# Kernel tuning notes

Measured on AMD Instinct MI355X. Metric: run time of the kernel, lower is better.

## Reference

```python
import jax, jax.numpy as jnp
import numpy as np

B, T, C = 4, 4096, 1024
NH, DH = 16, 128          # n_head, d_head = d_qkv // n_head
DQKV, DR = 2048, 256      # d_qkv, d_rank


def _uniform(key, shape, bound):
    return jax.random.uniform(key, shape, jnp.float32, -bound, bound)


def setup_inputs() -> dict:
    key = jax.random.key(0)
    k0, k1, k2, k3, k4 = jax.random.split(key, 5)
    # CastedLinear init: bound = sqrt(3) * 0.5 * in_features**-0.5 (same for w1, w2)
    b_qkv = (3 ** 0.5) * 0.5 * C ** (-0.5)
    b_proj = (3 ** 0.5) * 0.5 * DQKV ** (-0.5)
    return {
        "x": jax.random.normal(k0, (B, T, C), jnp.float32),
        "qkv_w1": _uniform(k1, (DR, C), b_qkv),
        "qkv_w2": _uniform(k2, (3 * DQKV, DR), b_qkv),
        "cproj_w1": _uniform(k3, (DR, DQKV), b_proj),
        "cproj_w2": _uniform(k4, (2 * C, DR), b_proj),
    }


def _rmsnorm(x):
    eps = jnp.finfo(x.dtype).eps  # F.rms_norm default eps
    return x * jax.lax.rsqrt(jnp.mean(x * x, axis=-1, keepdims=True) + eps)


def reference(x, qkv_w1, qkv_w2, cproj_w1, cproj_w2):
    Bx, Tx, Cx = x.shape
    # qkv projection with low-rank factorization + relu^2 activation between factors
    h = _rmsnorm(x) @ qkv_w1.T                      # [B,T,DR]
    h = jnp.square(jax.nn.relu(h))
    qkv = (h @ qkv_w2.T).reshape(Bx, Tx, 3 * NH, DH)
    q, k, v = jnp.split(qkv, 3, axis=2)             # each [B,T,NH,DH]
    q, k = _rmsnorm(q), _rmsnorm(k)

    # rotary embedding: half the head dim rotated, second quarter frequencies zero
    quarter = DH // 4
    freq = (1.0 / 1024.0) ** jnp.linspace(0.0, 1.0, quarter)
    freq = jnp.concatenate([freq, jnp.zeros(quarter, freq.dtype)])  # [DH//2]
    theta = jnp.arange(Tx, dtype=jnp.float32)[:, None] * freq[None, :]
    cos = jnp.cos(theta)[None, :, None, :]          # [1,T,1,DH//2]
    sin = jnp.sin(theta)[None, :, None, :]

    def rope(z):
        z1, z2 = jnp.split(z, 2, axis=-1)
        return jnp.concatenate([z1 * cos + z2 * sin, -z1 * sin + z2 * cos], axis=-1)

    q, k = rope(q), rope(k)

    # causal linear attention: sigmoid-gated cumulative sum over time
    y = jax.nn.relu(q) * jnp.cumsum(jax.nn.sigmoid(k) * v, axis=1)  # [B,T,NH,DH]
    y = y.reshape(Bx, Tx, NH * DH)

    # low-rank output projection (no activation), gated residual
    uv = (y @ cproj_w1.T) @ cproj_w2.T              # [B,T,2C]
    u, g = jnp.split(uv, 2, axis=-1)
    return x + u * jax.nn.silu(g)
```

## Files before the change

### kernel.cpp

```cpp
#include <hip/hip_runtime.h>
#include <hip/hip_bf16.h>

#define TB 4
#define TT 4096
#define TC 1024
#define TNH 16
#define TDH 128
#define TDQKV 2048
#define TDR 256
#define RB 4096
#define ROWS (TB*TT)
#define SLAB (RB*128)

typedef __attribute__((ext_vector_type(8))) short bfx8;
typedef __attribute__((ext_vector_type(4))) float fx4;
typedef __attribute__((address_space(1))) const unsigned char GAS;
typedef __attribute__((address_space(3))) unsigned char LAS;

__device__ __forceinline__ unsigned short f2b(float f) {
    unsigned int u = __float_as_uint(f);
    unsigned int r = (u + 0x7fffu + ((u >> 16) & 1u)) >> 16;
    return (unsigned short)r;
}
__device__ __forceinline__ float b2f(unsigned short h) {
    return __uint_as_float(((unsigned int)h) << 16);
}
__device__ __forceinline__ float sigm(float x) {
    return 1.0f / (1.0f + __expf(-x));
}
__device__ __forceinline__ int xcd_swz(int hw, int nwg) {
    int q = nwg >> 3;
    return (hw & 7) * q + (hw >> 3);
}

__global__ __launch_bounds__(256) void cvt_bf16(const float* __restrict__ in,
                                                unsigned short* __restrict__ out, int n) {
    int i = (blockIdx.x * 256 + threadIdx.x) * 4;
    if (i < n) {
        float4 v = *(const float4*)(in + i);
        out[i + 0] = f2b(v.x);
        out[i + 1] = f2b(v.y);
        out[i + 2] = f2b(v.z);
        out[i + 3] = f2b(v.w);
    }
}

__global__ __launch_bounds__(256) void rope_tab(float* __restrict__ ct, float* __restrict__ st) {
    int i = blockIdx.x * 256 + threadIdx.x;
    int t = i >> 5, j = i & 31;
    float fr = exp2f(-10.0f * (float)j / 31.0f);
    float th = (float)t * fr;
    ct[i] = cosf(th);
    st[i] = sinf(th);
}

__global__ __launch_bounds__(256) void rmsnorm_x(const float* __restrict__ x,
                                                 unsigned short* __restrict__ xn) {
    int row = blockIdx.x;
    int tid = threadIdx.x;
    float4 v = *(const float4*)(x + (size_t)row * TC + tid * 4);
    float ss = v.x * v.x + v.y * v.y + v.z * v.z + v.w * v.w;
    #pragma unroll
    for (int o = 32; o > 0; o >>= 1) ss += __shfl_xor(ss, o);
    __shared__ float red[4];
    if ((tid & 63) == 0) red[tid >> 6] = ss;
    __syncthreads();
    float tot = red[0] + red[1] + red[2] + red[3];
    float sc = rsqrtf(tot * (1.0f / TC) + 1.1920929e-7f);
    unsigned short* o = xn + (size_t)row * TC + tid * 4;
    o[0] = f2b(v.x * sc); o[1] = f2b(v.y * sc); o[2] = f2b(v.z * sc); o[3] = f2b(v.w * sc);
}

template <int EPI>
__global__ __launch_bounds__(256) void gemm_bt(const unsigned short* __restrict__ A, int lda,
                                               const unsigned short* __restrict__ Bm,
                                               unsigned short* __restrict__ C, int ldc,
                                               int N, int K) {
    __shared__ unsigned short As[2][128 * 32];
    __shared__ unsigned short Bs[2][128 * 32];
    const int m0 = blockIdx.y * 128;
    const int n0 = blockIdx.x * 128;
    const int tid = threadIdx.x;
    const int lane = tid & 63;
    const int w = tid >> 6;
    const int wr = w >> 1, wc = w & 1;
    const int r16 = lane & 15;
    const int kk = (lane >> 4) * 8;
    const int l4 = lane >> 2;
    const int c8 = (lane & 3) * 8;
    const int nk = K >> 5;
    fx4 acc[4][4] = {};

    auto stage = [&](int buf, int k0) {
        #pragma unroll
        for (int i = 0; i < 2; ++i) {
            int rr = (w + 4 * i) * 16 + l4;
            const unsigned short* ga = A + (size_t)(m0 + rr) * lda + k0 + c8;
            const unsigned short* gb = Bm + (size_t)(n0 + rr) * K + k0 + c8;
            __builtin_amdgcn_global_load_lds((GAS*)ga, (LAS*)&As[buf][(w + 4 * i) * 512], 16, 0, 0);
            __builtin_amdgcn_global_load_lds((GAS*)gb, (LAS*)&Bs[buf][(w + 4 * i) * 512], 16, 0, 0);
        }
    };

    stage(0, 0);
    __syncthreads();
    int buf = 0;
    for (int ks = 0; ks < nk; ++ks) {
        if (ks + 1 < nk) stage(buf ^ 1, (ks + 1) * 32);
        bfx8 af[4], bfr[4];
        #pragma unroll
        for (int mi = 0; mi < 4; mi++) af[mi] = *(const bfx8*)&As[buf][(wr * 64 + mi * 16 + r16) * 32 + kk];
        #pragma unroll
        for (int ni = 0; ni < 4; ni++) bfr[ni] = *(const bfx8*)&Bs[buf][(wc * 64 + ni * 16 + r16) * 32 + kk];
        #pragma unroll
        for (int mi = 0; mi < 4; mi++)
            #pragma unroll
            for (int ni = 0; ni < 4; ni++)
                acc[mi][ni] = __builtin_amdgcn_mfma_f32_16x16x32_bf16(af[mi], bfr[ni], acc[mi][ni], 0, 0, 0);
        __syncthreads();
        buf ^= 1;
    }

    const int rg = lane >> 4;
    #pragma unroll
    for (int mi = 0; mi < 4; mi++)
        #pragma unroll
        for (int ni = 0; ni < 4; ni++) {
            int col = n0 + wc * 64 + ni * 16 + r16;
            #pragma unroll
            for (int r = 0; r < 4; r++) {
                int row = m0 + wr * 64 + mi * 16 + rg * 4 + r;
                float v = acc[mi][ni][r];
                if (EPI == 1) { v = fmaxf(v, 0.0f); v *= v; }
                if (EPI == 2) {
                    int head = col >> 7;
                    C[(size_t)head * SLAB + (size_t)row * 128 + (col & 127)] = f2b(v);
                } else {
                    C[(size_t)row * ldc + col] = f2b(v);
                }
            }
        }
}

template <int EPI, int NX>
__global__ __launch_bounds__(256) void gemm_bt64(const unsigned short* __restrict__ A, int lda,
                                                 const unsigned short* __restrict__ Bm,
                                                 unsigned short* __restrict__ C, int ldc,
                                                 int K) {
    __shared__ unsigned short As[2][64 * 32];
    __shared__ unsigned short Bs[2][64 * 32];
    const int hw = blockIdx.y * gridDim.x + blockIdx.x;
    const int lg = xcd_swz(hw, gridDim.x * gridDim.y);
    const int n0 = (lg % NX) * 64;
    const int m0 = (lg / NX) * 64;
    const int tid = threadIdx.x;
    const int lane = tid & 63;
    const int w = tid >> 6;
    const int wr = w >> 1, wc = w & 1;
    const int r16 = lane & 15;
    const int kk = (lane >> 4) * 8;
    const int l4 = lane >> 2;
    const int c8 = (lane & 3) * 8;
    const int nk = K >> 5;
    fx4 acc[2][2] = {};

    auto stage = [&](int buf, int k0) {
        int rr = w * 16 + l4;
        const unsigned short* ga = A + (size_t)(m0 + rr) * lda + k0 + c8;
        const unsigned short* gb = Bm + (size_t)(n0 + rr) * K + k0 + c8;
        __builtin_amdgcn_global_load_lds((GAS*)ga, (LAS*)&As[buf][w * 512], 16, 0, 0);
        __builtin_amdgcn_global_load_lds((GAS*)gb, (LAS*)&Bs[buf][w * 512], 16, 0, 0);
    };

    stage(0, 0);
    __syncthreads();
    int buf = 0;
    for (int ks = 0; ks < nk; ++ks) {
        if (ks + 1 < nk) stage(buf ^ 1, (ks + 1) * 32);
        bfx8 af[2], bfr[2];
        #pragma unroll
        for (int mi = 0; mi < 2; mi++) af[mi] = *(const bfx8*)&As[buf][(wr * 32 + mi * 16 + r16) * 32 + kk];
        #pragma unroll
        for (int ni = 0; ni < 2; ni++) bfr[ni] = *(const bfx8*)&Bs[buf][(wc * 32 + ni * 16 + r16) * 32 + kk];
        #pragma unroll
        for (int mi = 0; mi < 2; mi++)
            #pragma unroll
            for (int ni = 0; ni < 2; ni++)
                acc[mi][ni] = __builtin_amdgcn_mfma_f32_16x16x32_bf16(af[mi], bfr[ni], acc[mi][ni], 0, 0, 0);
        __syncthreads();
        buf ^= 1;
    }

    const int rg = lane >> 4;
    #pragma unroll
    for (int mi = 0; mi < 2; mi++)
        #pragma unroll
        for (int ni = 0; ni < 2; ni++) {
            int col = n0 + wc * 32 + ni * 16 + r16;
            #pragma unroll
            for (int r = 0; r < 4; r++) {
                int row = m0 + wr * 32 + mi * 16 + rg * 4 + r;
                float v = acc[mi][ni][r];
                if (EPI == 1) { v = fmaxf(v, 0.0f); v *= v; }
                C[(size_t)row * ldc + col] = f2b(v);
            }
        }
}

__global__ __launch_bounds__(256) void gemm4f64(const unsigned short* __restrict__ A,
                                                const unsigned short* __restrict__ Wm,
                                                const float* __restrict__ x,
                                                float* __restrict__ out) {
    __shared__ unsigned short As[2][64 * 32];
    __shared__ unsigned short Bu[2][64 * 32];
    __shared__ unsigned short Bg[2][64 * 32];
    const int hw = blockIdx.y * gridDim.x + blockIdx.x;
    const int lg = xcd_swz(hw, gridDim.x * gridDim.y);
    const int n0 = (lg & 15) * 64;
    const int m0 = (lg >> 4) * 64;
    const int tid = threadIdx.x;
    const int lane = tid & 63;
    const int w = tid >> 6;
    const int wr = w >> 1, wc = w & 1;
    const int r16 = lane & 15;
    const int kk = (lane >> 4) * 8;
    const int l4 = lane >> 2;
    const int c8 = (lane & 3) * 8;
    fx4 accu[2][2] = {};
    fx4 accg[2][2] = {};

    auto stage = [&](int buf, int k0) {
        int rr = w * 16 + l4;
        const unsigned short* ga = A + (size_t)(m0 + rr) * TDR + k0 + c8;
        const unsigned short* gu = Wm + (size_t)(n0 + rr) * TDR + k0 + c8;
        const unsigned short* gg = Wm + (size_t)(1024 + n0 + rr) * TDR + k0 + c8;
        __builtin_amdgcn_global_load_lds((GAS*)ga, (LAS*)&As[buf][w * 512], 16, 0, 0);
        __builtin_amdgcn_global_load_lds((GAS*)gu, (LAS*)&Bu[buf][w * 512], 16, 0, 0);
        __builtin_amdgcn_global_load_lds((GAS*)gg, (LAS*)&Bg[buf][w * 512], 16, 0, 0);
    };

    stage(0, 0);
    __syncthreads();
    int buf = 0;
    for (int ks = 0; ks < 8; ++ks) {
        if (ks + 1 < 8) stage(buf ^ 1, (ks + 1) * 32);
        bfx8 af[2], bu[2], bg[2];
        #pragma unroll
        for (int mi = 0; mi < 2; mi++) af[mi] = *(const bfx8*)&As[buf][(wr * 32 + mi * 16 + r16) * 32 + kk];
        #pragma unroll
        for (int ni = 0; ni < 2; ni++) {
            bu[ni] = *(const bfx8*)&Bu[buf][(wc * 32 + ni * 16 + r16) * 32 + kk];
            bg[ni] = *(const bfx8*)&Bg[buf][(wc * 32 + ni * 16 + r16) * 32 + kk];
        }
        #pragma unroll
        for (int mi = 0; mi < 2; mi++)
            #pragma unroll
            for (int ni = 0; ni < 2; ni++) {
                accu[mi][ni] = __builtin_amdgcn_mfma_f32_16x16x32_bf16(af[mi], bu[ni], accu[mi][ni], 0, 0, 0);
                accg[mi][ni] = __builtin_amdgcn_mfma_f32_16x16x32_bf16(af[mi], bg[ni], accg[mi][ni], 0, 0, 0);
            }
        __syncthreads();
        buf ^= 1;
    }

    const int rg = lane >> 4;
    #pragma unroll
    for (int mi = 0; mi < 2; mi++)
        #pragma unroll
        for (int ni = 0; ni < 2; ni++) {
            int col = n0 + wc * 32 + ni * 16 + r16;
            #pragma unroll
            for (int r = 0; r < 4; r++) {
                int row = m0 + wr * 32 + mi * 16 + rg * 4 + r;
                float u = accu[mi][ni][r];
                float g = accg[mi][ni][r];
                size_t idx = (size_t)row * TC + col;
                out[idx] = x[idx] + u * (g * sigm(g));
            }
        }
}

__global__ __launch_bounds__(256) void post128(unsigned short* __restrict__ qkv,
                                               const float* __restrict__ ct,
                                               const float* __restrict__ st,
                                               float* __restrict__ part) {
    const int blk = blockIdx.x;
    const int mb = blk & 31, h = blk >> 5;
    const int w = threadIdx.x >> 6, lane = threadIdx.x & 63;
    unsigned short* qs = qkv + (size_t)h * SLAB;
    unsigned short* ks = qkv + (size_t)(16 + h) * SLAB;
    unsigned short* vs = qkv + (size_t)(32 + h) * SLAB;
    __shared__ float psum[4][2][128];
    const int d0 = lane * 2;
    const float sgn = (lane < 32) ? 1.0f : -1.0f;
    const int jh = lane & 31;

    #pragma unroll
    for (int half = 0; half < 2; ++half) {
        float a0 = 0.0f, a1 = 0.0f;
        for (int i = half * 16; i < half * 16 + 16; ++i) {
            int r = i * 4 + w;
            int t = mb * 128 + r;
            size_t off = (size_t)t * 128 + d0;
            ushort2 q2 = *(const ushort2*)(qs + off);
            ushort2 k2 = *(const ushort2*)(ks + off);
            float q0 = b2f(q2.x), q1 = b2f(q2.y);
            float k0 = b2f(k2.x), k1 = b2f(k2.y);
            float ssq = q0 * q0 + q1 * q1;
            float ssk = k0 * k0 + k1 * k1;
            #pragma unroll
            for (int o = 32; o > 0; o >>= 1) {
                ssq += __shfl_xor(ssq, o);
                ssk += __shfl_xor(ssk, o);
            }
            float qsc = rsqrtf(ssq * (1.0f / TDH) + 1.1920929e-7f);
            float ksc = rsqrtf(ssk * (1.0f / TDH) + 1.1920929e-7f);
            q0 *= qsc; q1 *= qsc; k0 *= ksc; k1 *= ksc;
            float qp0 = __shfl_xor(q0, 32), qp1 = __shfl_xor(q1, 32);
            float kp0 = __shfl_xor(k0, 32), kp1 = __shfl_xor(k1, 32);
            float c0 = 1.0f, c1 = 1.0f, s0 = 0.0f, s1 = 0.0f;
            if (jh < 16) {
                const float* cb = ct + t * 32 + jh * 2;
                const float* sb = st + t * 32 + jh * 2;
                c0 = cb[0]; c1 = cb[1]; s0 = sb[0] * sgn; s1 = sb[1] * sgn;
            }
            float qo0 = q0 * c0 + qp0 * s0;
            float qo1 = q1 * c1 + qp1 * s1;
            float ko0 = k0 * c0 + kp0 * s0;
            float ko1 = k1 * c1 + kp1 * s1;
            ushort2 v2 = *(const ushort2*)(vs + off);
            float p0 = sigm(ko0) * b2f(v2.x);
            float p1 = sigm(ko1) * b2f(v2.y);
            ushort2 qo; qo.x = f2b(qo0); qo.y = f2b(qo1);
            ushort2 po; po.x = f2b(p0);  po.y = f2b(p1);
            *(ushort2*)(qs + off) = qo;
            *(ushort2*)(ks + off) = po;
            a0 += p0; a1 += p1;
        }
        psum[w][half][d0] = a0;
        psum[w][half][d0 + 1] = a1;
    }
    __syncthreads();
    int seg = threadIdx.x >> 7, d = threadIdx.x & 127;
    float tot = psum[0][seg][d] + psum[1][seg][d] + psum[2][seg][d] + psum[3][seg][d];
    part[(size_t)(h * 64 + mb * 2 + seg) * 128 + d] = tot;
}

__global__ __launch_bounds__(256) void scanB(float* __restrict__ part) {
    int idx = blockIdx.x * 256 + threadIdx.x;
    int h = idx >> 7, d = idx & 127;
    float v[64];
    #pragma unroll
    for (int s = 0; s < 64; ++s) v[s] = part[((size_t)(h * 64 + s)) * 128 + d];
    float run = 0.0f;
    #pragma unroll
    for (int s = 0; s < 64; ++s) { float tv = v[s]; v[s] = run; run += tv; }
    #pragma unroll
    for (int s = 0; s < 64; ++s) part[((size_t)(h * 64 + s)) * 128 + d] = v[s];
}

__global__ __launch_bounds__(128) void scanC2(const unsigned short* __restrict__ qkv,
                                              const float* __restrict__ part,
                                              unsigned short* __restrict__ y) {
    int blk = blockIdx.x;
    int d = threadIdx.x;
    int s = blk & 63;
    int h = blk >> 6;
    const unsigned short* qp = qkv + (size_t)h * SLAB + (size_t)(s * 64) * 128 + d;
    const unsigned short* pp = qkv + (size_t)(16 + h) * SLAB + (size_t)(s * 64) * 128 + d;
    float sum = part[(size_t)blk * 128 + d];
    size_t yb = (size_t)(s * 64) * 2048 + (size_t)h * 128 + d;
    #pragma unroll 4
    for (int t = 0; t < 64; ++t) {
        sum += b2f(pp[t * 128]);
        float qv = b2f(qp[t * 128]);
        y[yb + (size_t)t * 2048] = f2b(fmaxf(qv, 0.0f) * sum);
    }
}

extern "C" void kernel_launch(void* const* d_in, const int* in_sizes, int n_in,
                              void* d_out, int out_size, void* d_ws, size_t ws_size,
                              hipStream_t stream) {
    (void)in_sizes; (void)n_in; (void)out_size; (void)ws_size;
    const float* x    = (const float*)d_in[0];
    const float* wq1  = (const float*)d_in[1];
    const float* wq2  = (const float*)d_in[2];
    const float* wc1  = (const float*)d_in[3];
    const float* wc2  = (const float*)d_in[4];
    float* out = (float*)d_out;

    char* ws = (char*)d_ws;
    size_t off = 0;
    auto alloc = [&](size_t bytes) -> void* {
        off = (off + 255) & ~(size_t)255;
        void* p = ws + off;
        off += bytes;
        return p;
    };
    char* pool = (char*)alloc((size_t)RB * 6144 * 2);
    unsigned short* qkvb = (unsigned short*)pool;
    unsigned short* xn   = (unsigned short*)pool;
    unsigned short* t1   = (unsigned short*)pool;
    unsigned short* hbuf = (unsigned short*)alloc((size_t)ROWS * TDR * 2);
    unsigned short* w1b  = (unsigned short*)alloc((size_t)TDR * TC * 2);
    unsigned short* w2b  = (unsigned short*)alloc((size_t)3 * TDQKV * TDR * 2);
    unsigned short* wp1b = (unsigned short*)alloc((size_t)TDR * TDQKV * 2);
    unsigned short* wp2b = (unsigned short*)alloc((size_t)2 * TC * TDR * 2);
    float* ct   = (float*)alloc((size_t)TT * 32 * 4);
    float* st   = (float*)alloc((size_t)TT * 32 * 4);
    float* part = (float*)alloc((size_t)TNH * 64 * 128 * 4);
    unsigned short* ybuf = (unsigned short*)d_out;

    cvt_bf16<<<(TDR * TC) / 1024, 256, 0, stream>>>(wq1, w1b, TDR * TC);
    cvt_bf16<<<(3 * TDQKV * TDR) / 1024, 256, 0, stream>>>(wq2, w2b, 3 * TDQKV * TDR);
    cvt_bf16<<<(TDR * TDQKV) / 1024, 256, 0, stream>>>(wc1, wp1b, TDR * TDQKV);
    cvt_bf16<<<(2 * TC * TDR) / 1024, 256, 0, stream>>>(wc2, wp2b, 2 * TC * TDR);
    rope_tab<<<(TT * 32) / 256, 256, 0, stream>>>(ct, st);

    rmsnorm_x<<<ROWS, 256, 0, stream>>>(x, xn);
    gemm_bt64<1, 4><<<dim3(TDR / 64, ROWS / 64), 256, 0, stream>>>(
        xn, TC, w1b, hbuf, TDR, TC);

    for (int b = 0; b < TB; ++b) {
        gemm_bt<2><<<dim3(6144 / 128, RB / 128), 256, 0, stream>>>(
            hbuf + (size_t)b * RB * TDR, TDR, w2b, qkvb, 0, 6144, TDR);
        post128<<<TNH * 32, 256, 0, stream>>>(qkvb, ct, st, part);
        scanB<<<(TNH * 128) / 256, 256, 0, stream>>>(part);
        scanC2<<<TNH * 64, 128, 0, stream>>>(qkvb, part, ybuf + (size_t)b * RB * 2048);
    }

    gemm_bt64<0, 4><<<dim3(TDR / 64, ROWS / 64), 256, 0, stream>>>(
        ybuf, 2048, wp1b, t1, TDR, TDQKV);
    gemm4f64<<<dim3(TC / 64, ROWS / 64), 256, 0, stream>>>(t1, wp2b, x, out);
}
```

Measured before the change: 425.3 us.

## Rework rope/gating and chunked scan kernels with wider vector accesses and finer segments

The post-processing kernel now gives each row to 16 lanes, each handling 8 elements as two 4-wide vectors covering both rope halves. This removes the cross-lane shuffles for the rotation and shortens the norm reduction. The number of scan segments doubles to 128 of 32 timesteps each. The final scan kernel uses 8-wide bf16 vector loads and stores, with each 16-lane group handling one segment, which should cut memory transaction overhead. The trade-offs are fewer blocks in the final scan and a longer serial carry scan over 128 segments.

```diff
diff --git a/kernel.cpp b/kernel.cpp
--- a/kernel.cpp
+++ b/kernel.cpp
@@ -11,6 +11,8 @@
 #define RB 4096
 #define ROWS (TB*TT)
 #define SLAB (RB*128)
+#define NSEG 128
+#define SEGT 32
 
 typedef __attribute__((ext_vector_type(8))) short bfx8;
 typedef __attribute__((ext_vector_type(4))) float fx4;
@@ -280,101 +282,136 @@
         }
 }
 
-__global__ __launch_bounds__(256) void post128(unsigned short* __restrict__ qkv,
-                                               const float* __restrict__ ct,
-                                               const float* __restrict__ st,
-                                               float* __restrict__ part) {
+__global__ __launch_bounds__(256) void post64(unsigned short* __restrict__ qkv,
+                                              const float* __restrict__ ct,
+                                              const float* __restrict__ st,
+                                              float* __restrict__ part) {
     const int blk = blockIdx.x;
-    const int mb = blk & 31, h = blk >> 5;
-    const int w = threadIdx.x >> 6, lane = threadIdx.x & 63;
+    const int tile = blk & 63, h = blk >> 6;
+    const int g = threadIdx.x >> 4, l16 = threadIdx.x & 15;
+    const int d0 = l16 * 4;
     unsigned short* qs = qkv + (size_t)h * SLAB;
     unsigned short* ks = qkv + (size_t)(16 + h) * SLAB;
     unsigned short* vs = qkv + (size_t)(32 + h) * SLAB;
-    __shared__ float psum[4][2][128];
-    const int d0 = lane * 2;
-    const float sgn = (lane < 32) ? 1.0f : -1.0f;
-    const int jh = lane & 31;
-
-    #pragma unroll
-    for (int half = 0; half < 2; ++half) {
-        float a0 = 0.0f, a1 = 0.0f;
-        for (int i = half * 16; i < half * 16 + 16; ++i) {
-            int r = i * 4 + w;
-            int t = mb * 128 + r;
-            size_t off = (size_t)t * 128 + d0;
-            ushort2 q2 = *(const ushort2*)(qs + off);
-            ushort2 k2 = *(const ushort2*)(ks + off);
-            float q0 = b2f(q2.x), q1 = b2f(q2.y);
-            float k0 = b2f(k2.x), k1 = b2f(k2.y);
-            float ssq = q0 * q0 + q1 * q1;
-            float ssk = k0 * k0 + k1 * k1;
-            #pragma unroll
-            for (int o = 32; o > 0; o >>= 1) {
-                ssq += __shfl_xor(ssq, o);
-                ssk += __shfl_xor(ssk, o);
-            }
-            float qsc = rsqrtf(ssq * (1.0f / TDH) + 1.1920929e-7f);
-            float ksc = rsqrtf(ssk * (1.0f / TDH) + 1.1920929e-7f);
-            q0 *= qsc; q1 *= qsc; k0 *= ksc; k1 *= ksc;
-            float qp0 = __shfl_xor(q0, 32), qp1 = __shfl_xor(q1, 32);
-            float kp0 = __shfl_xor(k0, 32), kp1 = __shfl_xor(k1, 32);
-            float c0 = 1.0f, c1 = 1.0f, s0 = 0.0f, s1 = 0.0f;
-            if (jh < 16) {
-                const float* cb = ct + t * 32 + jh * 2;
-                const float* sb = st + t * 32 + jh * 2;
-                c0 = cb[0]; c1 = cb[1]; s0 = sb[0] * sgn; s1 = sb[1] * sgn;
-            }
-            float qo0 = q0 * c0 + qp0 * s0;
-            float qo1 = q1 * c1 + qp1 * s1;
-            float ko0 = k0 * c0 + kp0 * s0;
-            float ko1 = k1 * c1 + kp1 * s1;
-            ushort2 v2 = *(const ushort2*)(vs + off);
-            float p0 = sigm(ko0) * b2f(v2.x);
-            float p1 = sigm(ko1) * b2f(v2.y);
-            ushort2 qo; qo.x = f2b(qo0); qo.y = f2b(qo1);
-            ushort2 po; po.x = f2b(p0);  po.y = f2b(p1);
-            *(ushort2*)(qs + off) = qo;
-            *(ushort2*)(ks + off) = po;
-            a0 += p0; a1 += p1;
-        }
-        psum[w][half][d0] = a0;
-        psum[w][half][d0 + 1] = a1;
+    __shared__ float psum[2][16][128];
+    float acc0[2][4] = {};
+    float acc1[2][4] = {};
+
+    #pragma unroll
+    for (int p = 0; p < 4; ++p) {
+        const int t = tile * 64 + p * 16 + g;
+        const size_t lo = (size_t)t * 128 + d0, hi = lo + 64;
+        ushort4 q1 = *(const ushort4*)(qs + lo);
+        ushort4 q2 = *(const ushort4*)(qs + hi);
+        ushort4 k1 = *(const ushort4*)(ks + lo);
+        ushort4 k2 = *(const ushort4*)(ks + hi);
+        float qa[8] = {b2f(q1.x), b2f(q1.y), b2f(q1.z), b2f(q1.w),
+                       b2f(q2.x), b2f(q2.y), b2f(q2.z), b2f(q2.w)};
+        float ka[8] = {b2f(k1.x), b2f(k1.y), b2f(k1.z), b2f(k1.w),
+                       b2f(k2.x), b2f(k2.y), b2f(k2.z), b2f(k2.w)};
+        float ssq = 0.0f, ssk = 0.0f;
+        #pragma unroll
+        for (int j = 0; j < 8; ++j) { ssq += qa[j] * qa[j]; ssk += ka[j] * ka[j]; }
+        #pragma unroll
+        for (int o = 8; o > 0; o >>= 1) {
+            ssq += __shfl_xor(ssq, o);
+            ssk += __shfl_xor(ssk, o);
+        }
+        float qsc = rsqrtf(ssq * (1.0f / TDH) + 1.1920929e-7f);
+        float ksc = rsqrtf(ssk * (1.0f / TDH) + 1.1920929e-7f);
+        float c[4], s[4];
+        if (l16 < 8) {
+            float4 cv = *(const float4*)(ct + t * 32 + d0);
+            float4 sv = *(const float4*)(st + t * 32 + d0);
+            c[0] = cv.x; c[1] = cv.y; c[2] = cv.z; c[3] = cv.w;
+            s[0] = sv.x; s[1] = sv.y; s[2] = sv.z; s[3] = sv.w;
+        } else {
+            c[0] = c[1] = c[2] = c[3] = 1.0f;
+            s[0] = s[1] = s[2] = s[3] = 0.0f;
+        }
+        ushort4 v1 = *(const ushort4*)(vs + lo);
+        ushort4 v2 = *(const ushort4*)(vs + hi);
+        float va[8] = {b2f(v1.x), b2f(v1.y), b2f(v1.z), b2f(v1.w),
+                       b2f(v2.x), b2f(v2.y), b2f(v2.z), b2f(v2.w)};
+        ushort4 qo1, qo2, po1, po2;
+        unsigned short* qo1p = (unsigned short*)&qo1;
+        unsigned short* qo2p = (unsigned short*)&qo2;
+        unsigned short* po1p = (unsigned short*)&po1;
+        unsigned short* po2p = (unsigned short*)&po2;
+        const int h2 = p >> 1;
+        #pragma unroll
+        for (int j = 0; j < 4; ++j) {
+            float z1q = qa[j] * qsc, z2q = qa[4 + j] * qsc;
+            float z1k = ka[j] * ksc, z2k = ka[4 + j] * ksc;
+            float qlo = z1q * c[j] + z2q * s[j];
+            float qhi = z2q * c[j] - z1q * s[j];
+            float klo = z1k * c[j] + z2k * s[j];
+            float khi = z2k * c[j] - z1k * s[j];
+            float plo = sigm(klo) * va[j];
+            float phi = sigm(khi) * va[4 + j];
+            qo1p[j] = f2b(qlo); qo2p[j] = f2b(qhi);
+            po1p[j] = f2b(plo); po2p[j] = f2b(phi);
+            acc0[h2][j] += plo;
+            acc1[h2][j] += phi;
+        }
+        *(ushort4*)(qs + lo) = qo1;
+        *(ushort4*)(qs + hi) = qo2;
+        *(ushort4*)(ks + lo) = po1;
+        *(ushort4*)(ks + hi) = po2;
+    }
+    #pragma unroll
+    for (int h2 = 0; h2 < 2; ++h2) {
+        *(float4*)&psum[h2][g][d0]      = *(float4*)acc0[h2];
+        *(float4*)&psum[h2][g][64 + d0] = *(float4*)acc1[h2];
     }
     __syncthreads();
-    int seg = threadIdx.x >> 7, d = threadIdx.x & 127;
-    float tot = psum[0][seg][d] + psum[1][seg][d] + psum[2][seg][d] + psum[3][seg][d];
-    part[(size_t)(h * 64 + mb * 2 + seg) * 128 + d] = tot;
-}
-
-__global__ __launch_bounds__(256) void scanB(float* __restrict__ part) {
+    const int h2 = threadIdx.x >> 7, d = threadIdx.x & 127;
+    float tot = 0.0f;
+    #pragma unroll
+    for (int gg = 0; gg < 16; ++gg) tot += psum[h2][gg][d];
+    part[((size_t)h * NSEG + tile * 2 + h2) * 128 + d] = tot;
+}
+
+__global__ __launch_bounds__(256) void scanB128(float* __restrict__ part) {
     int idx = blockIdx.x * 256 + threadIdx.x;
     int h = idx >> 7, d = idx & 127;
-    float v[64];
-    #pragma unroll
-    for (int s = 0; s < 64; ++s) v[s] = part[((size_t)(h * 64 + s)) * 128 + d];
     float run = 0.0f;
-    #pragma unroll
-    for (int s = 0; s < 64; ++s) { float tv = v[s]; v[s] = run; run += tv; }
-    #pragma unroll
-    for (int s = 0; s < 64; ++s) part[((size_t)(h * 64 + s)) * 128 + d] = v[s];
-}
-
-__global__ __launch_bounds__(128) void scanC2(const unsigned short* __restrict__ qkv,
+    #pragma unroll 8
+    for (int s = 0; s < NSEG; ++s) {
+        float* p = part + ((size_t)(h * NSEG + s)) * 128 + d;
+        float tv = *p;
+        *p = run;
+        run += tv;
+    }
+}
+
+__global__ __launch_bounds__(256) void scanC3(const unsigned short* __restrict__ qkv,
                                               const float* __restrict__ part,
                                               unsigned short* __restrict__ y) {
-    int blk = blockIdx.x;
-    int d = threadIdx.x;
-    int s = blk & 63;
-    int h = blk >> 6;
-    const unsigned short* qp = qkv + (size_t)h * SLAB + (size_t)(s * 64) * 128 + d;
-    const unsigned short* pp = qkv + (size_t)(16 + h) * SLAB + (size_t)(s * 64) * 128 + d;
-    float sum = part[(size_t)blk * 128 + d];
-    size_t yb = (size_t)(s * 64) * 2048 + (size_t)h * 128 + d;
+    const int bseg = blockIdx.x & 7, h = blockIdx.x >> 3;
+    const int g = threadIdx.x >> 4, l16 = threadIdx.x & 15;
+    const int seg = bseg * 16 + g;
+    const int d0 = l16 * 8;
+    const unsigned short* qp = qkv + (size_t)h * SLAB;
+    const unsigned short* pp = qkv + (size_t)(16 + h) * SLAB;
+    float sum[8];
+    const float* pb = part + ((size_t)(h * NSEG + seg)) * 128 + d0;
+    *(float4*)&sum[0] = *(const float4*)pb;
+    *(float4*)&sum[4] = *(const float4*)(pb + 4);
     #pragma unroll 4
-    for (int t = 0; t < 64; ++t) {
-        sum += b2f(pp[t * 128]);
-        float qv = b2f(qp[t * 128]);
-        y[yb + (size_t)t * 2048] = f2b(fmaxf(qv, 0.0f) * sum);
+    for (int i = 0; i < SEGT; ++i) {
+        int t = seg * SEGT + i;
+        size_t off = (size_t)t * 128 + d0;
+        bfx8 pv = *(const bfx8*)(pp + off);
+        bfx8 qv = *(const bfx8*)(qp + off);
+        bfx8 ov;
+        #pragma unroll
+        for (int j = 0; j < 8; ++j) {
+            sum[j] += b2f((unsigned short)pv[j]);
+            float q = b2f((unsigned short)qv[j]);
+            ov[j] = (short)f2b(fmaxf(q, 0.0f) * sum[j]);
+        }
+        *(bfx8*)(y + (size_t)t * 2048 + h * 128 + d0) = ov;
     }
 }
 
@@ -408,7 +445,7 @@
     unsigned short* wp2b = (unsigned short*)alloc((size_t)2 * TC * TDR * 2);
     float* ct   = (float*)alloc((size_t)TT * 32 * 4);
     float* st   = (float*)alloc((size_t)TT * 32 * 4);
-    float* part = (float*)alloc((size_t)TNH * 64 * 128 * 4);
+    float* part = (float*)alloc((size_t)TNH * NSEG * 128 * 4);
     unsigned short* ybuf = (unsigned short*)d_out;
 
     cvt_bf16<<<(TDR * TC) / 1024, 256, 0, stream>>>(wq1, w1b, TDR * TC);
@@ -424,9 +461,9 @@
     for (int b = 0; b < TB; ++b) {
         gemm_bt<2><<<dim3(6144 / 128, RB / 128), 256, 0, stream>>>(
             hbuf + (size_t)b * RB * TDR, TDR, w2b, qkvb, 0, 6144, TDR);
-        post128<<<TNH * 32, 256, 0, stream>>>(qkvb, ct, st, part);
-        scanB<<<(TNH * 128) / 256, 256, 0, stream>>>(part);
-        scanC2<<<TNH * 64, 128, 0, stream>>>(qkvb, part, ybuf + (size_t)b * RB * 2048);
+        post64<<<TNH * 64, 256, 0, stream>>>(qkvb, ct, st, part);
+        scanB128<<<(TNH * 128) / 256, 256, 0, stream>>>(part);
+        scanC3<<<TNH * 8, 256, 0, stream>>>(qkvb, part, ybuf + (size_t)b * RB * 2048);
     }
 
     gemm_bt64<0, 4><<<dim3(TDR / 64, ROWS / 64), 256, 0, stream>>>(
```

After: 383.1 us. 1.11x faster.
